# Optimization experiments

Hardware: AMD Instinct MI355X
Metric: run time of the kernel (lower is better)

## Reference

```python
import jax, jax.numpy as jnp
import numpy as np
from jax import lax

DIM = 128
DIM_PREV = 64
DIM_NEXT = 256
HEADS = 4
HID = int(DIM * 2.66)  # 340
B, H, W = 8, 128, 128


def conv2d(x, w, stride=1, pad=0, groups=1):
    return lax.conv_general_dilated(
        x, w, (stride, stride), ((pad, pad), (pad, pad)),
        feature_group_count=groups,
        dimension_numbers=('NCHW', 'OIHW', 'NCHW'))


def layernorm_c(x, w, b):
    # WithBias LayerNorm over channel dim (unbiased=False var), eps=1e-5
    mu = x.mean(axis=1, keepdims=True)
    var = ((x - mu) ** 2).mean(axis=1, keepdims=True)
    return (x - mu) / jnp.sqrt(var + 1e-5) * w[None, :, None, None] + b[None, :, None, None]


def pixel_shuffle(x, r=2):
    b, c, h, w = x.shape
    co = c // (r * r)
    return x.reshape(b, co, r, r, h, w).transpose(0, 1, 4, 2, 5, 3).reshape(b, co, h * r, w * r)


def attention(x, temperature, qkv_w, qkv_dw_w, proj_w, heads):
    b, c, h, w = x.shape
    qkv = conv2d(conv2d(x, qkv_w), qkv_dw_w, pad=1, groups=3 * c)
    q, k, v = jnp.split(qkv, 3, axis=1)
    rs = lambda t: t.reshape(b, heads, c // heads, h * w)
    q, k, v = rs(q), rs(k), rs(v)
    q = q / jnp.maximum(jnp.linalg.norm(q, axis=-1, keepdims=True), 1e-12)
    k = k / jnp.maximum(jnp.linalg.norm(k, axis=-1, keepdims=True), 1e-12)
    # channel-wise attention: [b, heads, c/h, c/h]
    attn = jax.nn.softmax(jnp.einsum('bhcn,bhdn->bhcd', q, k) * temperature[None], axis=-1)
    out = jnp.einsum('bhcd,bhdn->bhcn', attn, v).reshape(b, c, h, w)
    return conv2d(out, proj_w)


def ffn(x, pin_w, dw_w, pout_w):
    x = conv2d(x, pin_w)
    x = conv2d(x, dw_w, pad=1, groups=x.shape[1])
    x1, x2 = jnp.split(x, 2, axis=1)
    return conv2d(jax.nn.gelu(x1, approximate=False) * x2, pout_w)


def setup_inputs() -> dict:
    key = jax.random.key(0)
    ks = jax.random.split(key, 16)
    s = 0.05
    return {
        'x_main': jax.random.normal(ks[0], (B, DIM, H, W), jnp.float32),
        'x_prev': jax.random.normal(ks[1], (B, DIM_PREV, 2 * H, 2 * W), jnp.float32),
        'x_next': jax.random.normal(ks[2], (B, DIM_NEXT, H // 2, W // 2), jnp.float32),
        'alpha_down': jnp.float32(0.5),
        'alpha_up': jnp.float32(0.5),
        'down_w': jax.random.normal(ks[3], (DIM, DIM_PREV, 3, 3), jnp.float32) * s,
        'up_w': jax.random.normal(ks[4], (DIM * 4, DIM_NEXT, 1, 1), jnp.float32) * s,
        'norm1_w': jnp.ones((DIM,), jnp.float32),
        'norm1_b': jnp.zeros((DIM,), jnp.float32),
        'temperature': jnp.ones((HEADS, 1, 1), jnp.float32),
        'qkv_w': jax.random.normal(ks[5], (3 * DIM, DIM, 1, 1), jnp.float32) * s,
        'qkv_dw_w': jax.random.normal(ks[6], (3 * DIM, 1, 3, 3), jnp.float32) * s,
        'proj_w': jax.random.normal(ks[7], (DIM, DIM, 1, 1), jnp.float32) * s,
        'norm2_w': jnp.ones((DIM,), jnp.float32),
        'norm2_b': jnp.zeros((DIM,), jnp.float32),
        'ffn_in_w': jax.random.normal(ks[8], (2 * HID, DIM, 1, 1), jnp.float32) * s,
        'ffn_dw_w': jax.random.normal(ks[9], (2 * HID, 1, 3, 3), jnp.float32) * s,
        'ffn_out_w': jax.random.normal(ks[10], (DIM, HID, 1, 1), jnp.float32) * s,
    }


def reference(x_main, x_prev, x_next, alpha_down, alpha_up, down_w, up_w,
              norm1_w, norm1_b, temperature, qkv_w, qkv_dw_w, proj_w,
              norm2_w, norm2_b, ffn_in_w, ffn_dw_w, ffn_out_w):
    f = x_main + alpha_down * conv2d(x_prev, down_w, stride=2, pad=1)
    f = f + alpha_up * pixel_shuffle(conv2d(x_next, up_w))
    x = attention(layernorm_c(f, norm1_w, norm1_b), temperature, qkv_w, qkv_dw_w, proj_w, HEADS)
    x = x_main + x
    x = x + ffn(layernorm_c(x, norm2_w, norm2_b), ffn_in_w, ffn_dw_w, ffn_out_w)
    return x
```

## Files before the change

### kernel.cpp

```cpp
#include <hip/hip_runtime.h>
#include <hip/hip_bf16.h>
#include <math.h>

using bf16 = __hip_bfloat16;
#define DEV static __device__ __forceinline__

typedef float    fx4   __attribute__((ext_vector_type(4)));
typedef float    fx2   __attribute__((ext_vector_type(2)));
typedef short    s16x8 __attribute__((ext_vector_type(8)));
typedef short    s16x4 __attribute__((ext_vector_type(4)));
typedef __bf16   bfx8  __attribute__((ext_vector_type(8)));
typedef unsigned int u32x4 __attribute__((ext_vector_type(4)));

constexpr int BATCH = 8;
constexpr int NPIX  = 16384;
constexpr int KFF   = 352;
constexpr int MFI   = 768;
constexpr int H1S   = 704;

DEV float uu2f(unsigned short u) { return __uint_as_float(((unsigned)u) << 16); }
DEV unsigned short f2us(float f) { bf16 h = __float2bfloat16(f); return *(unsigned short*)&h; }
DEV float bl2f(bf16 v) { return __bfloat162float(v); }

constexpr size_t OFF_SL1   = 0;
constexpr size_t OFF_XNEXT = OFF_SL1;
constexpr size_t OFF_UP    = OFF_SL1 + 16777216;
constexpr size_t OFF_XPREV = OFF_SL1 + 50331648;
constexpr size_t SZ_SL1    = 184549376;
constexpr size_t OFF_SL2   = OFF_SL1 + SZ_SL1;
constexpr size_t OFF_SL3   = OFF_SL2 + 100663296;
constexpr size_t OFF_SL4   = OFF_SL3 + 33554432;
constexpr size_t OFF_SL5   = OFF_SL4 + 33554432;
constexpr size_t OFF_W     = OFF_SL5 + 33554432;
constexpr size_t OFF_WUP   = OFF_W;
constexpr size_t OFF_WQKV  = OFF_W +  262144;
constexpr size_t OFF_WPRJ  = OFF_W +  360448;
constexpr size_t OFF_WFIN  = OFF_W +  393216;
constexpr size_t OFF_WFOUT = OFF_W +  589824;
constexpr size_t OFF_WTAP  = OFF_W +  679936;
constexpr size_t OFF_ZP    = OFF_W +  827392;
constexpr size_t OFF_NBUF  = OFF_W +  974848;
constexpr size_t OFF_S     = OFF_W +  983040;

__global__ void conv_pad(const float* __restrict__ src, bf16* __restrict__ dst,
                         int Rs, int Cs, int Rd, int Cd)
{
    int n = Rd * Cd;
    for (int i = blockIdx.x * 256 + threadIdx.x; i < n; i += gridDim.x * 256) {
        int r = i / Cd, c = i % Cd;
        dst[i] = (r < Rs && c < Cs) ? __float2bfloat16(src[r * Cs + c]) : bf16(0.f);
    }
}

__global__ void wtap_prep(const float* __restrict__ src, bf16* __restrict__ dst)
{
    int i = blockIdx.x * 256 + threadIdx.x;
    if (i >= 9 * 128 * 64) return;
    int tap = i >> 13, rm = i & 8191, co = rm >> 6, ci = rm & 63;
    dst[i] = __float2bfloat16(src[(co * 64 + ci) * 9 + tap]);
}

__global__ void h1_padzero(bf16* __restrict__ h1)
{
    size_t idx = (size_t)blockIdx.x * 256 + threadIdx.x;
    if (idx >= (size_t)BATCH * NPIX * 24) return;
    size_t n = idx / 24;
    int j = (int)(idx % 24);
    int col = (j < 12) ? 340 + j : 680 + j;
    h1[n * H1S + col] = bf16(0.f);
}

__global__ __launch_bounds__(256) void transpose_c2p(
    const float* __restrict__ in, bf16* __restrict__ out, int C, int HW)
{
    __shared__ float ts[32][33];
    int hw0 = blockIdx.x * 32, c0 = blockIdx.y * 32, b = blockIdx.z;
    int rl = threadIdx.x >> 5, cl = threadIdx.x & 31;
#pragma unroll
    for (int i = 0; i < 4; i++)
        ts[rl + i * 8][cl] = in[((size_t)b * C + c0 + rl + i * 8) * HW + hw0 + cl];
    __syncthreads();
#pragma unroll
    for (int i = 0; i < 4; i++)
        out[((size_t)b * HW + hw0 + rl + i * 8) * C + c0 + cl] =
            __float2bfloat16(ts[cl][rl + i * 8]);
}

template <int EPI>
__global__ __launch_bounds__(256) void gemm_mfma(
    const bf16* __restrict__ Act, const bf16* __restrict__ Wt,
    int K, int Npb, int Mtrue, int Mstride,
    bf16* __restrict__ outB,
    const float* __restrict__ xmain, bf16* __restrict__ x_out,
    const float* __restrict__ nw, const float* __restrict__ nb,
    const bf16* __restrict__ xres, float* __restrict__ outF)
{
    __shared__ short As[128 * 32];
    __shared__ short Bs[128 * 32];
    const int t = threadIdx.x;
    const int w = t >> 6, lane = t & 63;
    const int wr = w >> 1, wc = w & 1;
    const int lr = lane & 15, lg = lane >> 4;
    const int n0 = blockIdx.x * 128;
    const int m0 = blockIdx.y * 128;
    const int b  = blockIdx.z;
    const bf16* Abase = Act + (size_t)b * Npb * K;

    fx4 acc[4][4];
#pragma unroll
    for (int i = 0; i < 4; i++)
#pragma unroll
        for (int j = 0; j < 4; j++) acc[i][j] = fx4{0.f, 0.f, 0.f, 0.f};

    const int f0 = w * 128 + lane, f1 = f0 + 64;
    const int r0 = f0 >> 2, c0 = (f0 & 3) * 8;
    const int r1 = f1 >> 2, c1 = (f1 & 3) * 8;

    for (int ks = 0; ks < K; ks += 32) {
        __builtin_amdgcn_global_load_lds(
            (const __attribute__((address_space(1))) void*)(Abase + (size_t)(n0 + r0) * K + ks + c0),
            (__attribute__((address_space(3))) void*)(As + w * 1024), 16, 0, 0);
        __builtin_amdgcn_global_load_lds(
            (const __attribute__((address_space(1))) void*)(Abase + (size_t)(n0 + r1) * K + ks + c1),
            (__attribute__((address_space(3))) void*)(As + w * 1024 + 512), 16, 0, 0);
        __builtin_amdgcn_global_load_lds(
            (const __attribute__((address_space(1))) void*)(Wt + (size_t)(m0 + r0) * K + ks + c0),
            (__attribute__((address_space(3))) void*)(Bs + w * 1024), 16, 0, 0);
        __builtin_amdgcn_global_load_lds(
            (const __attribute__((address_space(1))) void*)(Wt + (size_t)(m0 + r1) * K + ks + c1),
            (__attribute__((address_space(3))) void*)(Bs + w * 1024 + 512), 16, 0, 0);
        __syncthreads();
        bfx8 af[4], bw[4];
#pragma unroll
        for (int mi = 0; mi < 4; mi++)
            af[mi] = __builtin_bit_cast(bfx8,
                *(const s16x8*)&As[(wr * 64 + mi * 16 + lr) * 32 + lg * 8]);
#pragma unroll
        for (int ni = 0; ni < 4; ni++)
            bw[ni] = __builtin_bit_cast(bfx8,
                *(const s16x8*)&Bs[(wc * 64 + ni * 16 + lr) * 32 + lg * 8]);
#pragma unroll
        for (int mi = 0; mi < 4; mi++)
#pragma unroll
            for (int ni = 0; ni < 4; ni++)
                acc[mi][ni] = __builtin_amdgcn_mfma_f32_16x16x32_bf16(
                    af[mi], bw[ni], acc[mi][ni], 0, 0, 0);
        __syncthreads();
    }

    if (EPI == 0) {
#pragma unroll
        for (int mi = 0; mi < 4; mi++)
#pragma unroll
            for (int ni = 0; ni < 4; ni++) {
                int co = m0 + wc * 64 + ni * 16 + lr;
                if (co < Mtrue) {
#pragma unroll
                    for (int r = 0; r < 4; r++) {
                        int px = n0 + wr * 64 + mi * 16 + lg * 4 + r;
                        outB[((size_t)b * Npb + px) * Mstride + co] =
                            __float2bfloat16(acc[mi][ni][r]);
                    }
                }
            }
    } else if (EPI == 1) {
        float xv[4][4][4];
#pragma unroll
        for (int mi = 0; mi < 4; mi++)
#pragma unroll
            for (int ni = 0; ni < 4; ni++) {
                int co = wc * 64 + ni * 16 + lr;
                fx4 x4 = *(const fx4*)&xmain[((size_t)b * 128 + co) * 16384 +
                                             n0 + wr * 64 + mi * 16 + lg * 4];
#pragma unroll
                for (int r = 0; r < 4; r++) xv[mi][ni][r] = x4[r] + acc[mi][ni][r];
            }
        __shared__ float ps[2][128];
        __shared__ float pss[2][128];
#pragma unroll
        for (int mi = 0; mi < 4; mi++)
#pragma unroll
            for (int r = 0; r < 4; r++) {
                float s = 0.f, s2 = 0.f;
#pragma unroll
                for (int ni = 0; ni < 4; ni++) {
                    float v = xv[mi][ni][r]; s += v; s2 += v * v;
                }
#pragma unroll
                for (int m = 1; m < 16; m <<= 1) {
                    s  += __shfl_xor(s, m);
                    s2 += __shfl_xor(s2, m);
                }
                if (lr == 0) {
                    int row = wr * 64 + mi * 16 + lg * 4 + r;
                    ps[wc][row] = s; pss[wc][row] = s2;
                }
            }
        __syncthreads();
        float nwv[4], nbv[4];
#pragma unroll
        for (int ni = 0; ni < 4; ni++) {
            int co = wc * 64 + ni * 16 + lr;
            nwv[ni] = nw[co]; nbv[ni] = nb[co];
        }
#pragma unroll
        for (int mi = 0; mi < 4; mi++)
#pragma unroll
            for (int r = 0; r < 4; r++) {
                int row = wr * 64 + mi * 16 + lg * 4 + r;
                float s  = ps[0][row] + ps[1][row];
                float s2 = pss[0][row] + pss[1][row];
                float mu = s * (1.f / 128.f);
                float var = s2 * (1.f / 128.f) - mu * mu;
                float rstd = rsqrtf(var + 1e-5f);
                size_t px = (size_t)b * 16384 + n0 + row;
#pragma unroll
                for (int ni = 0; ni < 4; ni++) {
                    int co = wc * 64 + ni * 16 + lr;
                    float v = xv[mi][ni][r];
                    x_out[px * 128 + co] = __float2bfloat16(v);
                    outB[px * 128 + co] = __float2bfloat16((v - mu) * rstd * nwv[ni] + nbv[ni]);
                }
            }
    } else {
#pragma unroll
        for (int mi = 0; mi < 4; mi++)
#pragma unroll
            for (int ni = 0; ni < 4; ni++) {
                int co = wc * 64 + ni * 16 + lr;
                int pxb = n0 + wr * 64 + mi * 16 + lg * 4;
                fx4 o;
#pragma unroll
                for (int r = 0; r < 4; r++)
                    o[r] = acc[mi][ni][r] +
                           bl2f(xres[((size_t)b * 16384 + pxb + r) * 128 + co]);
                *(fx4*)&outF[((size_t)b * 128 + co) * 16384 + pxb] = o;
            }
    }
}

template <int REMAP>
__global__ __launch_bounds__(256) void gemm_mloop(
    const bf16* __restrict__ Act, const bf16* __restrict__ Wt,
    int nM, int Mtrue, int Mstride, bf16* __restrict__ outB)
{
    __shared__ short As[16384];
    __shared__ short Bs[16384];
    const int t = threadIdx.x;
    const int w = t >> 6, lane = t & 63;
    const int wr = w >> 1, wc = w & 1;
    const int lr = lane & 15, lg = lane >> 4;
    const int n0 = blockIdx.x * 128;
    const int b  = blockIdx.y;
    const short* Abase = (const short*)Act + (size_t)b * NPIX * 128;

#pragma unroll
    for (int i = 0; i < 8; i++) {
        int chunk = i * 256 + w * 64 + lane;
        int kb = chunk >> 9, row = (chunk >> 2) & 127, c8 = chunk & 3;
        __builtin_amdgcn_global_load_lds(
            (const __attribute__((address_space(1))) void*)
                (Abase + (size_t)(n0 + row) * 128 + kb * 32 + c8 * 8),
            (__attribute__((address_space(3))) void*)(As + i * 2048 + w * 512), 16, 0, 0);
    }

    for (int mt = 0; mt < nM; mt++) {
#pragma unroll
        for (int i = 0; i < 8; i++) {
            int chunk = i * 256 + w * 64 + lane;
            int kb = chunk >> 9, row = (chunk >> 2) & 127, c8 = chunk & 3;
            __builtin_amdgcn_global_load_lds(
                (const __attribute__((address_space(1))) void*)
                    ((const short*)Wt + (size_t)(mt * 128 + row) * 128 + kb * 32 + c8 * 8),
                (__attribute__((address_space(3))) void*)(Bs + i * 2048 + w * 512), 16, 0, 0);
        }
        __syncthreads();
        fx4 acc[4][4];
#pragma unroll
        for (int i = 0; i < 4; i++)
#pragma unroll
            for (int j = 0; j < 4; j++) acc[i][j] = fx4{0.f, 0.f, 0.f, 0.f};
#pragma unroll
        for (int ks = 0; ks < 4; ks++) {
            bfx8 af[4], bw[4];
#pragma unroll
            for (int mi = 0; mi < 4; mi++)
                af[mi] = __builtin_bit_cast(bfx8,
                    *(const s16x8*)&As[ks * 4096 + (wr * 64 + mi * 16 + lr) * 32 + lg * 8]);
#pragma unroll
            for (int ni = 0; ni < 4; ni++)
                bw[ni] = __builtin_bit_cast(bfx8,
                    *(const s16x8*)&Bs[ks * 4096 + (wc * 64 + ni * 16 + lr) * 32 + lg * 8]);
#pragma unroll
            for (int mi = 0; mi < 4; mi++)
#pragma unroll
                for (int ni = 0; ni < 4; ni++)
                    acc[mi][ni] = __builtin_amdgcn_mfma_f32_16x16x32_bf16(
                        af[mi], bw[ni], acc[mi][ni], 0, 0, 0);
        }
        __syncthreads();
#pragma unroll
        for (int mi = 0; mi < 4; mi++)
#pragma unroll
            for (int ni = 0; ni < 4; ni++) {
                int co = mt * 128 + wc * 64 + ni * 16 + lr;
                if (co < Mtrue) {
                    int cd = (REMAP && co >= 340) ? co + 12 : co;
#pragma unroll
                    for (int r = 0; r < 4; r++) {
                        int px = n0 + wr * 64 + mi * 16 + lg * 4 + r;
                        outB[((size_t)b * NPIX + px) * Mstride + cd] =
                            __float2bfloat16(acc[mi][ni][r]);
                    }
                }
            }
    }
}

__global__ __launch_bounds__(256) void down_mfma_ln(
    const bf16* __restrict__ xprev_pm,
    const float* __restrict__ xmain,
    const bf16* __restrict__ up_pm,
    const bf16* __restrict__ wtap,
    const float* __restrict__ alpha_d, const float* __restrict__ alpha_u,
    const float* __restrict__ n1w, const float* __restrict__ n1b,
    const bf16* __restrict__ zeropage,
    bf16* __restrict__ y1)
{
    __shared__ short As[128 * 64];
    __shared__ short Bs[128 * 64];
    __shared__ float ps[2][128];
    __shared__ float pss[2][128];
    const int t = threadIdx.x;
    const int w = t >> 6, lane = t & 63;
    const int wr = w >> 1, wc = w & 1;
    const int lr = lane & 15, lg = lane >> 4;
    const int y = blockIdx.x;
    const int b = blockIdx.y;

    const int srow0 = 32 * w + (lane >> 3);
    const int sci8  = lane & 7;
    const short* wtbase = (const short*)wtap;

    fx4 acc[4][4];
#pragma unroll
    for (int i = 0; i < 4; i++)
#pragma unroll
        for (int j = 0; j < 4; j++) acc[i][j] = fx4{0.f, 0.f, 0.f, 0.f};

#pragma unroll
    for (int tap = 0; tap < 9; tap++) {
        const int dy = tap / 3, dx = tap % 3;
        const int iy = 2 * y - 1 + dy;
        const bool rowok = (iy >= 0) && (iy < 256);
        const short* arow = (const short*)xprev_pm +
                            (((size_t)b * 65536 + (size_t)iy * 256) * 64);
#pragma unroll
        for (int i = 0; i < 4; i++) {
            int row = srow0 + 8 * i;
            int ix = 2 * row - 1 + dx;
            const short* src = (rowok && ix >= 0 && ix < 256)
                                 ? (arow + (size_t)ix * 64 + sci8 * 8)
                                 : (const short*)zeropage;
            __builtin_amdgcn_global_load_lds(
                (const __attribute__((address_space(1))) void*)src,
                (__attribute__((address_space(3))) void*)(As + w * 2048 + i * 512), 16, 0, 0);
            __builtin_amdgcn_global_load_lds(
                (const __attribute__((address_space(1))) void*)
                    (wtbase + tap * 8192 + w * 2048 + i * 512 + lane * 8),
                (__attribute__((address_space(3))) void*)(Bs + w * 2048 + i * 512), 16, 0, 0);
        }
        __syncthreads();
        bfx8 af[4][2], bw[4][2];
#pragma unroll
        for (int mi = 0; mi < 4; mi++)
#pragma unroll
            for (int ks = 0; ks < 2; ks++)
                af[mi][ks] = __builtin_bit_cast(bfx8,
                    *(const s16x8*)&As[(wr * 64 + mi * 16 + lr) * 64 + ks * 32 + lg * 8]);
#pragma unroll
        for (int ni = 0; ni < 4; ni++)
#pragma unroll
            for (int ks = 0; ks < 2; ks++)
                bw[ni][ks] = __builtin_bit_cast(bfx8,
                    *(const s16x8*)&Bs[(wc * 64 + ni * 16 + lr) * 64 + ks * 32 + lg * 8]);
#pragma unroll
        for (int mi = 0; mi < 4; mi++)
#pragma unroll
            for (int ni = 0; ni < 4; ni++)
#pragma unroll
                for (int ks = 0; ks < 2; ks++)
                    acc[mi][ni] = __builtin_amdgcn_mfma_f32_16x16x32_bf16(
                        af[mi][ks], bw[ni][ks], acc[mi][ni], 0, 0, 0);
        __syncthreads();
    }

    const float ad = alpha_d[0], au = alpha_u[0];
    const int n2base = (y >> 1) * 64;
    const int chb2 = (y & 1) * 2;
    float fv[4][4][4];
#pragma unroll
    for (int mi = 0; mi < 4; mi++) {
        const int x0 = wr * 64 + mi * 16 + lg * 4;
#pragma unroll
        for (int ni = 0; ni < 4; ni++) {
            const int co = wc * 64 + ni * 16 + lr;
            fx4 xm = *(const fx4*)&xmain[(((size_t)b * 128 + co) * 128 + y) * 128 + x0];
            const short* uprow = (const short*)up_pm +
                ((size_t)b * 4096 + n2base + (x0 >> 1)) * 512 + co * 4 + chb2;
            unsigned up01 = *(const unsigned*)uprow;
            unsigned up23 = *(const unsigned*)(uprow + 512);
            fv[mi][ni][0] = xm[0] + ad * acc[mi][ni][0] + au * uu2f((unsigned short)(up01 & 0xffff));
            fv[mi][ni][1] = xm[1] + ad * acc[mi][ni][1] + au * uu2f((unsigned short)(up01 >> 16));
            fv[mi][ni][2] = xm[2] + ad * acc[mi][ni][2] + au * uu2f((unsigned short)(up23 & 0xffff));
            fv[mi][ni][3] = xm[3] + ad * acc[mi][ni][3] + au * uu2f((unsigned short)(up23 >> 16));
        }
    }
#pragma unroll
    for (int mi = 0; mi < 4; mi++)
#pragma unroll
        for (int r = 0; r < 4; r++) {
            float s = 0.f, s2 = 0.f;
#pragma unroll
            for (int ni = 0; ni < 4; ni++) {
                float v = fv[mi][ni][r]; s += v; s2 += v * v;
            }
#pragma unroll
            for (int m = 1; m < 16; m <<= 1) {
                s  += __shfl_xor(s, m);
                s2 += __shfl_xor(s2, m);
            }
            if (lr == 0) {
                int row = wr * 64 + mi * 16 + lg * 4 + r;
                ps[wc][row] = s; pss[wc][row] = s2;
            }
        }
    __syncthreads();
    float nwv[4], nbv[4];
#pragma unroll
    for (int ni = 0; ni < 4; ni++) {
        int co = wc * 64 + ni * 16 + lr;
        nwv[ni] = n1w[co]; nbv[ni] = n1b[co];
    }
#pragma unroll
    for (int mi = 0; mi < 4; mi++)
#pragma unroll
        for (int r = 0; r < 4; r++) {
            int row = wr * 64 + mi * 16 + lg * 4 + r;
            float s  = ps[0][row] + ps[1][row];
            float s2 = pss[0][row] + pss[1][row];
            float mu = s * (1.f / 128.f);
            float var = s2 * (1.f / 128.f) - mu * mu;
            float rstd = rsqrtf(var + 1e-5f);
            size_t px = (size_t)b * 16384 + (size_t)y * 128 + row;
#pragma unroll
            for (int ni = 0; ni < 4; ni++) {
                int co = wc * 64 + ni * 16 + lr;
                ((short*)y1)[px * 128 + co] =
                    (short)f2us((fv[mi][ni][r] - mu) * rstd * nwv[ni] + nbv[ni]);
            }
        }
}

DEV void dw_accum(const short* __restrict__ L, const float* __restrict__ swb,
                  int x, int yh, int lofs, fx2 acc[4][4])
{
    fx2 wreg[9][4];
#pragma unroll
    for (int tap = 0; tap < 9; tap++)
#pragma unroll
        for (int k = 0; k < 4; k++)
            wreg[tap][k] = *(const fx2*)&swb[tap * 32 + lofs + 2 * k];
#pragma unroll
    for (int yy = 0; yy < 4; yy++)
#pragma unroll
        for (int k = 0; k < 4; k++) acc[yy][k] = fx2{0.f, 0.f};
#pragma unroll
    for (int r = 0; r < 6; r++) {
        fx2 rv[3][4];
#pragma unroll
        for (int dxp = 0; dxp < 3; dxp++) {
            s16x8 raw = *(const s16x8*)&L[((yh * 4 + r) * 34 + x + dxp) * 40 + lofs];
            u32x4 u = __builtin_bit_cast(u32x4, raw);
#pragma unroll
            for (int k = 0; k < 4; k++)
                rv[dxp][k] = fx2{__uint_as_float(u[k] << 16),
                                 __uint_as_float(u[k] & 0xffff0000u)};
        }
#pragma unroll
        for (int yy = 0; yy < 4; yy++) {
            int dy = r - yy;
            if (dy < 0 || dy > 2) continue;
#pragma unroll
            for (int dx = 0; dx < 3; dx++)
#pragma unroll
                for (int k = 0; k < 4; k++)
                    acc[yy][k] += rv[dx][k] * wreg[dy * 3 + dx][k];
        }
    }
}

template <int GATE, int QKNORM>
__global__ __launch_bounds__(256) void dw_conv(
    const bf16* __restrict__ in, const float* __restrict__ w,
    bf16* __restrict__ out, float* __restrict__ nbuf)
{
    constexpr int CHST  = GATE ? 704 : 384;
    constexpr int CHOST = GATE ? 352 : 384;
    __shared__ short L1[13600];
    __shared__ short L2[GATE ? 13600 : 8];
    __shared__ float sw1[288];
    __shared__ float sw2[GATE ? 288 : 8];
    __shared__ float snorm[32];
    const int t = threadIdx.x;
    const int x = t & 31, chg = (t >> 5) & 3, yh = t >> 7;
    const int cg = blockIdx.y, b = blockIdx.z;
    const int x0 = (blockIdx.x & 3) * 32, y0 = (blockIdx.x >> 2) * 8;

    if (QKNORM && t < 32) snorm[t] = 0.f;
    if (GATE) {
        for (int i = t; i < 288; i += 256) {
            int c = i & 31, tap = i >> 5;
            int cr = cg * 32 + c;
            sw1[i] = (cr < 340) ? w[cr * 9 + tap] : 0.f;
            sw2[i] = (cr < 340) ? w[(cr + 340) * 9 + tap] : 0.f;
        }
    } else {
        for (int i = t; i < 288; i += 256) {
            int c = i & 31, tap = i >> 5;
            sw1[i] = w[(cg * 32 + c) * 9 + tap];
        }
    }
    const short* bin = (const short*)in + (size_t)b * NPIX * CHST + cg * 32;
    const int NCHK = GATE ? 2720 : 1360;
    for (int id = t; id < NCHK; id += 256) {
        int half = 0, idd = id;
        if (GATE && idd >= 1360) { half = 1; idd -= 1360; }
        int row = idd / 136, rm = idd % 136, pos = rm >> 2, c8 = rm & 3;
        int gy = y0 - 1 + row, gx = x0 - 1 + pos;
        s16x8 v = s16x8{0, 0, 0, 0, 0, 0, 0, 0};
        if (gy >= 0 && gy < 128 && gx >= 0 && gx < 128)
            v = *(const s16x8*)(bin + ((size_t)(gy << 7) + gx) * CHST + half * 352 + c8 * 8);
        short* dst = (GATE && half) ? L2 : L1;
        *(s16x8*)&dst[(row * 34 + pos) * 40 + c8 * 8] = v;
    }
    __syncthreads();

    const int lofs = chg * 8;
    fx2 a1[4][4];
    dw_accum(L1, sw1, x, yh, lofs, a1);
    if (GATE) {
#pragma unroll
        for (int yy = 0; yy < 4; yy++)
#pragma unroll
            for (int k = 0; k < 4; k++) {
                fx2 v = a1[yy][k];
#pragma unroll
                for (int e = 0; e < 2; e++) {
                    float xx = v[e];
                    float x2 = xx * xx;
                    float mzz = xx * fmaf(-0.1029432f, x2, -2.3022082f);
                    float un = exp2f(mzz);
                    v[e] = xx * __builtin_amdgcn_rcpf(1.f + un);
                }
                a1[yy][k] = v;
            }
        fx2 a2[4][4];
        dw_accum(L2, sw2, x, yh, lofs, a2);
#pragma unroll
        for (int yy = 0; yy < 4; yy++)
#pragma unroll
            for (int k = 0; k < 4; k++) a1[yy][k] *= a2[yy][k];
    }

    if (QKNORM && cg < 8) {
        fx2 sq[4];
#pragma unroll
        for (int k = 0; k < 4; k++) {
            sq[k] = fx2{0.f, 0.f};
#pragma unroll
            for (int yy = 0; yy < 4; yy++) sq[k] += a1[yy][k] * a1[yy][k];
        }
#pragma unroll
        for (int m = 1; m < 32; m <<= 1)
#pragma unroll
            for (int k = 0; k < 4; k++) {
                sq[k][0] += __shfl_xor(sq[k][0], m);
                sq[k][1] += __shfl_xor(sq[k][1], m);
            }
        if (x == 0) {
#pragma unroll
            for (int k = 0; k < 4; k++) {
                atomicAdd(&snorm[chg * 8 + 2 * k],     sq[k][0]);
                atomicAdd(&snorm[chg * 8 + 2 * k + 1], sq[k][1]);
            }
        }
    }

#pragma unroll
    for (int yy = 0; yy < 4; yy++) {
        s16x8 pk;
#pragma unroll
        for (int k = 0; k < 4; k++) {
            pk[2 * k]     = (short)f2us(a1[yy][k][0]);
            pk[2 * k + 1] = (short)f2us(a1[yy][k][1]);
        }
        *(s16x8*)((short*)out + (((size_t)b * NPIX) + ((y0 + yh * 4 + yy) << 7) + x0 + x) * CHOST
                  + cg * 32 + chg * 8) = pk;
    }

    if (QKNORM) {
        __syncthreads();
        if (cg < 8 && t < 32)
            atomicAdd(&nbuf[b * 256 + cg * 32 + t], snorm[t]);
    }
}

__global__ __launch_bounds__(256) void scores(const bf16* __restrict__ qkv,
                                              float* __restrict__ S)
{
    __shared__ short qs[256 * 40];
    __shared__ short ks2[256 * 40];
    const int t = threadIdx.x;
    const int bh = blockIdx.x, b = bh >> 2, h = bh & 3;
    const int n0 = blockIdx.y * 256;
    {
        const short* src = (const short*)qkv + ((size_t)(b * 16384 + n0 + t)) * 384 + h * 32;
#pragma unroll
        for (int i = 0; i < 4; i++) {
            *(s16x8*)&qs[t * 40 + i * 8]  = *(const s16x8*)(src + i * 8);
            *(s16x8*)&ks2[t * 40 + i * 8] = *(const s16x8*)(src + 128 + i * 8);
        }
    }
    __syncthreads();
    const int i2 = t >> 4, j16 = t & 15;
    float a00 = 0.f, a01 = 0.f, a10 = 0.f, a11 = 0.f;
    for (int n = 0; n < 256; n++) {
        unsigned qq = *(const unsigned*)&qs[n * 40 + i2 * 2];
        unsigned kk = *(const unsigned*)&ks2[n * 40 + j16 * 2];
        float q0 = uu2f((unsigned short)(qq & 0xffff)), q1 = uu2f((unsigned short)(qq >> 16));
        float k0 = uu2f((unsigned short)(kk & 0xffff)), k1 = uu2f((unsigned short)(kk >> 16));
        a00 = fmaf(q0, k0, a00); a01 = fmaf(q0, k1, a01);
        a10 = fmaf(q1, k0, a10); a11 = fmaf(q1, k1, a11);
    }
    float* base = S + (size_t)bh * 1024;
    atomicAdd(&base[(i2 * 2 + 0) * 32 + j16 * 2 + 0], a00);
    atomicAdd(&base[(i2 * 2 + 0) * 32 + j16 * 2 + 1], a01);
    atomicAdd(&base[(i2 * 2 + 1) * 32 + j16 * 2 + 0], a10);
    atomicAdd(&base[(i2 * 2 + 1) * 32 + j16 * 2 + 1], a11);
}

__global__ void softmax_k(float* __restrict__ S, const float* __restrict__ nbuf,
                          const float* __restrict__ temp)
{
    __shared__ float invk[32];
    int bh = blockIdx.x, b = bh >> 2, h = bh & 3, i = threadIdx.x;
    invk[i] = 1.f / fmaxf(sqrtf(nbuf[b * 256 + 128 + h * 32 + i]), 1e-12f);
    __syncthreads();
    float ti = temp[h] / fmaxf(sqrtf(nbuf[b * 256 + h * 32 + i]), 1e-12f);
    float* row = S + (size_t)bh * 1024 + i * 32;
    float vals[32], m = -1e30f;
#pragma unroll
    for (int j = 0; j < 32; j++) { vals[j] = row[j] * ti * invk[j]; m = fmaxf(m, vals[j]); }
    float s = 0.f;
#pragma unroll
    for (int j = 0; j < 32; j++) { vals[j] = expf(vals[j] - m); s += vals[j]; }
    float r = 1.f / s;
#pragma unroll
    for (int j = 0; j < 32; j++) row[j] = vals[j] * r;
}

__global__ __launch_bounds__(256) void attnapply(const bf16* __restrict__ qkv,
                                                 const float* __restrict__ S,
                                                 bf16* __restrict__ atto)
{
    __shared__ float sa[1024];
    const int t = threadIdx.x;
    const int bh = blockIdx.x, b = bh >> 2, h = bh & 3;
    const int n0 = blockIdx.y * 1024;
    for (int i = t; i < 1024; i += 256) sa[i] = S[(size_t)bh * 1024 + i];
    __syncthreads();
#pragma unroll
    for (int pp = 0; pp < 4; pp++) {
        int n = n0 + (t << 2) + pp;
        const short* vs = (const short*)qkv + ((size_t)(b * 16384) + n) * 384 + 256 + h * 32;
        float v[32];
#pragma unroll
        for (int i = 0; i < 4; i++) {
            s16x8 vv = *(const s16x8*)(vs + i * 8);
#pragma unroll
            for (int e = 0; e < 8; e++) v[i * 8 + e] = uu2f((unsigned short)vv[e]);
        }
        short ov[32];
#pragma unroll
        for (int c = 0; c < 32; c++) {
            const fx4* row = (const fx4*)&sa[c * 32];
            float a = 0.f;
#pragma unroll
            for (int d4 = 0; d4 < 8; d4++) {
                fx4 w4 = row[d4];
                a += w4[0] * v[d4 * 4] + w4[1] * v[d4 * 4 + 1] +
                     w4[2] * v[d4 * 4 + 2] + w4[3] * v[d4 * 4 + 3];
            }
            ov[c] = (short)f2us(a);
        }
        short* dst = (short*)atto + ((size_t)(b * 16384) + n) * 128 + h * 32;
#pragma unroll
        for (int i = 0; i < 4; i++) *(s16x8*)(dst + i * 8) = *(s16x8*)&ov[i * 8];
    }
}

extern "C" void kernel_launch(void* const* d_in, const int* in_sizes, int n_in,
                              void* d_out, int out_size, void* d_ws, size_t ws_size,
                              hipStream_t stream)
{
    const float* x_main      = (const float*)d_in[0];
    const float* x_prev      = (const float*)d_in[1];
    const float* x_next      = (const float*)d_in[2];
    const float* alpha_down  = (const float*)d_in[3];
    const float* alpha_up    = (const float*)d_in[4];
    const float* down_w      = (const float*)d_in[5];
    const float* up_w        = (const float*)d_in[6];
    const float* norm1_w     = (const float*)d_in[7];
    const float* norm1_b     = (const float*)d_in[8];
    const float* temperature = (const float*)d_in[9];
    const float* qkv_w       = (const float*)d_in[10];
    const float* qkv_dw_w    = (const float*)d_in[11];
    const float* proj_w      = (const float*)d_in[12];
    const float* norm2_w     = (const float*)d_in[13];
    const float* norm2_b     = (const float*)d_in[14];
    const float* ffn_in_w    = (const float*)d_in[15];
    const float* ffn_dw_w    = (const float*)d_in[16];
    const float* ffn_out_w   = (const float*)d_in[17];
    float* out = (float*)d_out;
    (void)in_sizes; (void)n_in; (void)out_size; (void)ws_size;

    char* ws = (char*)d_ws;
    bf16* xnext_pm = (bf16*)(ws + OFF_XNEXT);
    bf16* up_pm    = (bf16*)(ws + OFF_UP);
    bf16* xprev_pm = (bf16*)(ws + OFF_XPREV);
    bf16* qkv_a    = (bf16*)(ws + OFF_SL1);
    bf16* h1       = (bf16*)(ws + OFF_SL1);
    bf16* qkv_b    = (bf16*)(ws + OFF_SL2);
    bf16* gbuf     = (bf16*)(ws + OFF_SL2);
    bf16* y1       = (bf16*)(ws + OFF_SL3);
    bf16* atto     = (bf16*)(ws + OFF_SL3);
    bf16* x_pm     = (bf16*)(ws + OFF_SL4);
    bf16* y2       = (bf16*)(ws + OFF_SL5);
    bf16* Wup      = (bf16*)(ws + OFF_WUP);
    bf16* Wqkv     = (bf16*)(ws + OFF_WQKV);
    bf16* Wprj     = (bf16*)(ws + OFF_WPRJ);
    bf16* Wfin     = (bf16*)(ws + OFF_WFIN);
    bf16* Wfout    = (bf16*)(ws + OFF_WFOUT);
    bf16* Wtap     = (bf16*)(ws + OFF_WTAP);
    bf16* zpage    = (bf16*)(ws + OFF_ZP);
    float* nbuf    = (float*)(ws + OFF_NBUF);
    float* Sbuf    = (float*)(ws + OFF_S);

    hipMemsetAsync(nbuf, 0, 8192 + 131072, stream);
    hipMemsetAsync(zpage, 0, 256, stream);

    conv_pad<<<dim3(512), 256, 0, stream>>>(up_w, Wup, 512, 256, 512, 256);
    conv_pad<<<dim3(192), 256, 0, stream>>>(qkv_w, Wqkv, 384, 128, 384, 128);
    conv_pad<<<dim3(64), 256, 0, stream>>>(proj_w, Wprj, 128, 128, 128, 128);
    conv_pad<<<dim3(384), 256, 0, stream>>>(ffn_in_w, Wfin, 680, 128, MFI, 128);
    conv_pad<<<dim3(176), 256, 0, stream>>>(ffn_out_w, Wfout, 128, 340, 128, KFF);
    wtap_prep<<<dim3(288), 256, 0, stream>>>(down_w, Wtap);

    transpose_c2p<<<dim3(128, 8, BATCH), 256, 0, stream>>>(x_next, xnext_pm, 256, 4096);
    transpose_c2p<<<dim3(2048, 2, BATCH), 256, 0, stream>>>(x_prev, xprev_pm, 64, 65536);

    gemm_mfma<0><<<dim3(32, 4, BATCH), 256, 0, stream>>>(
        xnext_pm, Wup, 256, 4096, 512, 512, up_pm,
        nullptr, nullptr, nullptr, nullptr, nullptr, nullptr);

    down_mfma_ln<<<dim3(128, BATCH), 256, 0, stream>>>(
        xprev_pm, x_main, up_pm, Wtap, alpha_down, alpha_up, norm1_w, norm1_b,
        zpage, y1);

    gemm_mloop<0><<<dim3(128, BATCH), 256, 0, stream>>>(y1, Wqkv, 3, 384, 384, qkv_a);

    dw_conv<0, 1><<<dim3(64, 12, BATCH), 256, 0, stream>>>(qkv_a, qkv_dw_w, qkv_b, nbuf);

    scores<<<dim3(32, 64), 256, 0, stream>>>(qkv_b, Sbuf);
    softmax_k<<<dim3(32), 32, 0, stream>>>(Sbuf, nbuf, temperature);
    attnapply<<<dim3(32, 16), 256, 0, stream>>>(qkv_b, Sbuf, atto);

    gemm_mfma<1><<<dim3(128, 1, BATCH), 256, 0, stream>>>(
        atto, Wprj, 128, NPIX, 128, 128, y2,
        x_main, x_pm, norm2_w, norm2_b, nullptr, nullptr);

    h1_padzero<<<dim3((BATCH * NPIX * 24 + 255) / 256), 256, 0, stream>>>(h1);
    gemm_mloop<1><<<dim3(128, BATCH), 256, 0, stream>>>(y2, Wfin, 6, 680, H1S, h1);

    dw_conv<1, 0><<<dim3(64, 11, BATCH), 256, 0, stream>>>(h1, ffn_dw_w, gbuf, nullptr);

    gemm_mfma<2><<<dim3(128, 1, BATCH), 256, 0, stream>>>(
        gbuf, Wfout, KFF, NPIX, 128, 128, nullptr,
        nullptr, nullptr, nullptr, nullptr, x_pm, out);
}
```

Measured before the change: 615.7 us.

## Fold attention matrix into projection weights and trim FFN staging

```diff
diff --git a/kernel.cpp b/kernel.cpp
--- a/kernel.cpp
+++ b/kernel.cpp
@@ -41,6 +41,7 @@
 constexpr size_t OFF_ZP    = OFF_W +  827392;
 constexpr size_t OFF_NBUF  = OFF_W +  974848;
 constexpr size_t OFF_S     = OFF_W +  983040;
+constexpr size_t OFF_W2    = OFF_W + 1114112;
 
 __global__ void conv_pad(const float* __restrict__ src, bf16* __restrict__ dst,
                          int Rs, int Cs, int Rd, int Cd)
@@ -60,16 +61,6 @@
     dst[i] = __float2bfloat16(src[(co * 64 + ci) * 9 + tap]);
 }
 
-__global__ void h1_padzero(bf16* __restrict__ h1)
-{
-    size_t idx = (size_t)blockIdx.x * 256 + threadIdx.x;
-    if (idx >= (size_t)BATCH * NPIX * 24) return;
-    size_t n = idx / 24;
-    int j = (int)(idx % 24);
-    int col = (j < 12) ? 340 + j : 680 + j;
-    h1[n * H1S + col] = bf16(0.f);
-}
-
 __global__ __launch_bounds__(256) void transpose_c2p(
     const float* __restrict__ in, bf16* __restrict__ out, int C, int HW)
 {
@@ -89,7 +80,7 @@
 template <int EPI>
 __global__ __launch_bounds__(256) void gemm_mfma(
     const bf16* __restrict__ Act, const bf16* __restrict__ Wt,
-    int K, int Npb, int Mtrue, int Mstride,
+    int K, int Npb, int Mtrue, int Mstride, int Astride, int Aoff, int WtBS,
     bf16* __restrict__ outB,
     const float* __restrict__ xmain, bf16* __restrict__ x_out,
     const float* __restrict__ nw, const float* __restrict__ nb,
@@ -104,7 +95,8 @@
     const int n0 = blockIdx.x * 128;
     const int m0 = blockIdx.y * 128;
     const int b  = blockIdx.z;
-    const bf16* Abase = Act + (size_t)b * Npb * K;
+    const bf16* Abase = Act + (size_t)b * Npb * Astride + Aoff;
+    const bf16* Wtb   = Wt + (size_t)b * WtBS;
 
     fx4 acc[4][4];
 #pragma unroll
@@ -118,16 +110,16 @@
 
     for (int ks = 0; ks < K; ks += 32) {
         __builtin_amdgcn_global_load_lds(
-            (const __attribute__((address_space(1))) void*)(Abase + (size_t)(n0 + r0) * K + ks + c0),
+            (const __attribute__((address_space(1))) void*)(Abase + (size_t)(n0 + r0) * Astride + ks + c0),
             (__attribute__((address_space(3))) void*)(As + w * 1024), 16, 0, 0);
         __builtin_amdgcn_global_load_lds(
-            (const __attribute__((address_space(1))) void*)(Abase + (size_t)(n0 + r1) * K + ks + c1),
+            (const __attribute__((address_space(1))) void*)(Abase + (size_t)(n0 + r1) * Astride + ks + c1),
             (__attribute__((address_space(3))) void*)(As + w * 1024 + 512), 16, 0, 0);
         __builtin_amdgcn_global_load_lds(
-            (const __attribute__((address_space(1))) void*)(Wt + (size_t)(m0 + r0) * K + ks + c0),
+            (const __attribute__((address_space(1))) void*)(Wtb + (size_t)(m0 + r0) * K + ks + c0),
             (__attribute__((address_space(3))) void*)(Bs + w * 1024), 16, 0, 0);
         __builtin_amdgcn_global_load_lds(
-            (const __attribute__((address_space(1))) void*)(Wt + (size_t)(m0 + r1) * K + ks + c1),
+            (const __attribute__((address_space(1))) void*)(Wtb + (size_t)(m0 + r1) * K + ks + c1),
             (__attribute__((address_space(3))) void*)(Bs + w * 1024 + 512), 16, 0, 0);
         __syncthreads();
         bfx8 af[4], bw[4];
@@ -311,6 +303,19 @@
                         int px = n0 + wr * 64 + mi * 16 + lg * 4 + r;
                         outB[((size_t)b * NPIX + px) * Mstride + cd] =
                             __float2bfloat16(acc[mi][ni][r]);
+                    }
+                    if (REMAP && co >= 340 && co < 352) {
+#pragma unroll
+                        for (int r = 0; r < 4; r++) {
+                            int px = n0 + wr * 64 + mi * 16 + lg * 4 + r;
+                            outB[((size_t)b * NPIX + px) * Mstride + co] = bf16(0.f);
+                        }
+                    }
+                } else if (REMAP && co < 692) {
+#pragma unroll
+                    for (int r = 0; r < 4; r++) {
+                        int px = n0 + wr * 64 + mi * 16 + lg * 4 + r;
+                        outB[((size_t)b * NPIX + px) * Mstride + co + 12] = bf16(0.f);
                     }
                 }
             }
@@ -465,53 +470,48 @@
 DEV void dw_accum(const short* __restrict__ L, const float* __restrict__ swb,
                   int x, int yh, int lofs, fx2 acc[4][4])
 {
-    fx2 wreg[9][4];
-#pragma unroll
-    for (int tap = 0; tap < 9; tap++)
-#pragma unroll
-        for (int k = 0; k < 4; k++)
-            wreg[tap][k] = *(const fx2*)&swb[tap * 32 + lofs + 2 * k];
 #pragma unroll
     for (int yy = 0; yy < 4; yy++)
 #pragma unroll
         for (int k = 0; k < 4; k++) acc[yy][k] = fx2{0.f, 0.f};
 #pragma unroll
-    for (int r = 0; r < 6; r++) {
-        fx2 rv[3][4];
-#pragma unroll
-        for (int dxp = 0; dxp < 3; dxp++) {
-            s16x8 raw = *(const s16x8*)&L[((yh * 4 + r) * 34 + x + dxp) * 40 + lofs];
+    for (int dxp = 0; dxp < 3; dxp++) {
+        fx2 rv[6][4];
+#pragma unroll
+        for (int r = 0; r < 6; r++) {
+            s16x8 raw = *(const s16x8*)&L[((yh * 4 + r) * 34 + x + dxp) * 44 + lofs];
             u32x4 u = __builtin_bit_cast(u32x4, raw);
 #pragma unroll
             for (int k = 0; k < 4; k++)
-                rv[dxp][k] = fx2{__uint_as_float(u[k] << 16),
-                                 __uint_as_float(u[k] & 0xffff0000u)};
-        }
-#pragma unroll
-        for (int yy = 0; yy < 4; yy++) {
-            int dy = r - yy;
-            if (dy < 0 || dy > 2) continue;
-#pragma unroll
-            for (int dx = 0; dx < 3; dx++)
+                rv[r][k] = fx2{__uint_as_float(u[k] << 16),
+                               __uint_as_float(u[k] & 0xffff0000u)};
+        }
+#pragma unroll
+        for (int dy = 0; dy < 3; dy++) {
+            fx2 wv[4];
+#pragma unroll
+            for (int k = 0; k < 4; k++)
+                wv[k] = *(const fx2*)&swb[(dy * 3 + dxp) * 32 + lofs + 2 * k];
+#pragma unroll
+            for (int yy = 0; yy < 4; yy++)
 #pragma unroll
                 for (int k = 0; k < 4; k++)
-                    acc[yy][k] += rv[dx][k] * wreg[dy * 3 + dx][k];
+                    acc[yy][k] += rv[yy + dy][k] * wv[k];
         }
     }
 }
 
 template <int GATE, int QKNORM>
-__global__ __launch_bounds__(256) void dw_conv(
+__global__ __launch_bounds__(256, 4) void dw_conv(
     const bf16* __restrict__ in, const float* __restrict__ w,
     bf16* __restrict__ out, float* __restrict__ nbuf)
 {
     constexpr int CHST  = GATE ? 704 : 384;
     constexpr int CHOST = GATE ? 352 : 384;
-    __shared__ short L1[13600];
-    __shared__ short L2[GATE ? 13600 : 8];
+    __shared__ short L[10 * 34 * 44];
     __shared__ float sw1[288];
     __shared__ float sw2[GATE ? 288 : 8];
-    __shared__ float snorm[32];
+    __shared__ float snorm[QKNORM ? 32 : 8];
     const int t = threadIdx.x;
     const int x = t & 31, chg = (t >> 5) & 3, yh = t >> 7;
     const int cg = blockIdx.y, b = blockIdx.z;
@@ -532,45 +532,51 @@
         }
     }
     const short* bin = (const short*)in + (size_t)b * NPIX * CHST + cg * 32;
-    const int NCHK = GATE ? 2720 : 1360;
-    for (int id = t; id < NCHK; id += 256) {
-        int half = 0, idd = id;
-        if (GATE && idd >= 1360) { half = 1; idd -= 1360; }
-        int row = idd / 136, rm = idd % 136, pos = rm >> 2, c8 = rm & 3;
-        int gy = y0 - 1 + row, gx = x0 - 1 + pos;
-        s16x8 v = s16x8{0, 0, 0, 0, 0, 0, 0, 0};
-        if (gy >= 0 && gy < 128 && gx >= 0 && gx < 128)
-            v = *(const s16x8*)(bin + ((size_t)(gy << 7) + gx) * CHST + half * 352 + c8 * 8);
-        short* dst = (GATE && half) ? L2 : L1;
-        *(s16x8*)&dst[(row * 34 + pos) * 40 + c8 * 8] = v;
-    }
+    auto stage = [&](int hofs) {
+        for (int id = t; id < 1360; id += 256) {
+            int row = id / 136, rm = id % 136, pos = rm >> 2, c8 = rm & 3;
+            int gy = y0 - 1 + row, gx = x0 - 1 + pos;
+            s16x8 v = s16x8{0, 0, 0, 0, 0, 0, 0, 0};
+            if (gy >= 0 && gy < 128 && gx >= 0 && gx < 128)
+                v = *(const s16x8*)(bin + ((size_t)(gy << 7) + gx) * CHST + hofs + c8 * 8);
+            *(s16x8*)&L[(row * 34 + pos) * 44 + c8 * 8] = v;
+        }
+    };
+    stage(0);
     __syncthreads();
 
     const int lofs = chg * 8;
     fx2 a1[4][4];
-    dw_accum(L1, sw1, x, yh, lofs, a1);
+    dw_accum(L, sw1, x, yh, lofs, a1);
+
     if (GATE) {
+        s16x8 p1[4];
 #pragma unroll
         for (int yy = 0; yy < 4; yy++)
 #pragma unroll
             for (int k = 0; k < 4; k++) {
-                fx2 v = a1[yy][k];
 #pragma unroll
                 for (int e = 0; e < 2; e++) {
-                    float xx = v[e];
+                    float xx = a1[yy][k][e];
                     float x2 = xx * xx;
                     float mzz = xx * fmaf(-0.1029432f, x2, -2.3022082f);
                     float un = exp2f(mzz);
-                    v[e] = xx * __builtin_amdgcn_rcpf(1.f + un);
+                    p1[yy][2 * k + e] = (short)f2us(xx * __builtin_amdgcn_rcpf(1.f + un));
                 }
-                a1[yy][k] = v;
-            }
+            }
+        __syncthreads();
+        stage(352);
+        __syncthreads();
         fx2 a2[4][4];
-        dw_accum(L2, sw2, x, yh, lofs, a2);
+        dw_accum(L, sw2, x, yh, lofs, a2);
 #pragma unroll
         for (int yy = 0; yy < 4; yy++)
 #pragma unroll
-            for (int k = 0; k < 4; k++) a1[yy][k] *= a2[yy][k];
+            for (int k = 0; k < 4; k++) {
+                fx2 g = fx2{uu2f((unsigned short)p1[yy][2 * k]),
+                            uu2f((unsigned short)p1[yy][2 * k + 1])};
+                a1[yy][k] = g * a2[yy][k];
+            }
     }
 
     if (QKNORM && cg < 8) {
@@ -670,44 +676,38 @@
     for (int j = 0; j < 32; j++) row[j] = vals[j] * r;
 }
 
-__global__ __launch_bounds__(256) void attnapply(const bf16* __restrict__ qkv,
-                                                 const float* __restrict__ S,
-                                                 bf16* __restrict__ atto)
-{
-    __shared__ float sa[1024];
-    const int t = threadIdx.x;
-    const int bh = blockIdx.x, b = bh >> 2, h = bh & 3;
-    const int n0 = blockIdx.y * 1024;
-    for (int i = t; i < 1024; i += 256) sa[i] = S[(size_t)bh * 1024 + i];
+__global__ __launch_bounds__(256) void attn_fold(
+    const bf16* __restrict__ Wprj, const float* __restrict__ S, bf16* __restrict__ W2)
+{
+    __shared__ float sS[4096];
+    const int b = blockIdx.x, t = threadIdx.x;
+    for (int i = t; i < 4096; i += 256) sS[i] = S[b * 4096 + i];
     __syncthreads();
-#pragma unroll
-    for (int pp = 0; pp < 4; pp++) {
-        int n = n0 + (t << 2) + pp;
-        const short* vs = (const short*)qkv + ((size_t)(b * 16384) + n) * 384 + 256 + h * 32;
-        float v[32];
-#pragma unroll
-        for (int i = 0; i < 4; i++) {
-            s16x8 vv = *(const s16x8*)(vs + i * 8);
-#pragma unroll
-            for (int e = 0; e < 8; e++) v[i * 8 + e] = uu2f((unsigned short)vv[e]);
-        }
-        short ov[32];
-#pragma unroll
-        for (int c = 0; c < 32; c++) {
-            const fx4* row = (const fx4*)&sa[c * 32];
+    const int co = t >> 1, jh = t & 1;
+    const short* prow = (const short*)Wprj + co * 128 + jh * 64;
+    float p[64];
+#pragma unroll
+    for (int i = 0; i < 8; i++) {
+        s16x8 v = *(const s16x8*)(prow + i * 8);
+#pragma unroll
+        for (int e = 0; e < 8; e++) p[i * 8 + e] = uu2f((unsigned short)v[e]);
+    }
+    short outv[64];
+#pragma unroll
+    for (int h2 = 0; h2 < 2; h2++) {
+        const int h = jh * 2 + h2;
+        const float* Sh = &sS[h * 1024];
+#pragma unroll 4
+        for (int d = 0; d < 32; d++) {
             float a = 0.f;
 #pragma unroll
-            for (int d4 = 0; d4 < 8; d4++) {
-                fx4 w4 = row[d4];
-                a += w4[0] * v[d4 * 4] + w4[1] * v[d4 * 4 + 1] +
-                     w4[2] * v[d4 * 4 + 2] + w4[3] * v[d4 * 4 + 3];
-            }
-            ov[c] = (short)f2us(a);
-        }
-        short* dst = (short*)atto + ((size_t)(b * 16384) + n) * 128 + h * 32;
-#pragma unroll
-        for (int i = 0; i < 4; i++) *(s16x8*)(dst + i * 8) = *(s16x8*)&ov[i * 8];
-    }
+            for (int c = 0; c < 32; c++) a = fmaf(p[h2 * 32 + c], Sh[c * 32 + d], a);
+            outv[h2 * 32 + d] = (short)f2us(a);
+        }
+    }
+    short* dst = (short*)W2 + (size_t)b * 16384 + co * 128 + jh * 64;
+#pragma unroll
+    for (int i = 0; i < 8; i++) *(s16x8*)(dst + i * 8) = *(s16x8*)&outv[i * 8];
 }
 
 extern "C" void kernel_launch(void* const* d_in, const int* in_sizes, int n_in,
@@ -744,7 +744,6 @@
     bf16* qkv_b    = (bf16*)(ws + OFF_SL2);
     bf16* gbuf     = (bf16*)(ws + OFF_SL2);
     bf16* y1       = (bf16*)(ws + OFF_SL3);
-    bf16* atto     = (bf16*)(ws + OFF_SL3);
     bf16* x_pm     = (bf16*)(ws + OFF_SL4);
     bf16* y2       = (bf16*)(ws + OFF_SL5);
     bf16* Wup      = (bf16*)(ws + OFF_WUP);
@@ -756,6 +755,7 @@
     bf16* zpage    = (bf16*)(ws + OFF_ZP);
     float* nbuf    = (float*)(ws + OFF_NBUF);
     float* Sbuf    = (float*)(ws + OFF_S);
+    bf16* W2buf    = (bf16*)(ws + OFF_W2);
 
     hipMemsetAsync(nbuf, 0, 8192 + 131072, stream);
     hipMemsetAsync(zpage, 0, 256, stream);
@@ -771,7 +771,7 @@
     transpose_c2p<<<dim3(2048, 2, BATCH), 256, 0, stream>>>(x_prev, xprev_pm, 64, 65536);
 
     gemm_mfma<0><<<dim3(32, 4, BATCH), 256, 0, stream>>>(
-        xnext_pm, Wup, 256, 4096, 512, 512, up_pm,
+        xnext_pm, Wup, 256, 4096, 512, 512, 256, 0, 0, up_pm,
         nullptr, nullptr, nullptr, nullptr, nullptr, nullptr);
 
     down_mfma_ln<<<dim3(128, BATCH), 256, 0, stream>>>(
@@ -784,18 +784,17 @@
 
     scores<<<dim3(32, 64), 256, 0, stream>>>(qkv_b, Sbuf);
     softmax_k<<<dim3(32), 32, 0, stream>>>(Sbuf, nbuf, temperature);
-    attnapply<<<dim3(32, 16), 256, 0, stream>>>(qkv_b, Sbuf, atto);
+    attn_fold<<<dim3(BATCH), 256, 0, stream>>>(Wprj, Sbuf, W2buf);
 
     gemm_mfma<1><<<dim3(128, 1, BATCH), 256, 0, stream>>>(
-        atto, Wprj, 128, NPIX, 128, 128, y2,
+        qkv_b, W2buf, 128, NPIX, 128, 128, 384, 256, 16384, y2,
         x_main, x_pm, norm2_w, norm2_b, nullptr, nullptr);
 
-    h1_padzero<<<dim3((BATCH * NPIX * 24 + 255) / 256), 256, 0, stream>>>(h1);
     gemm_mloop<1><<<dim3(128, BATCH), 256, 0, stream>>>(y2, Wfin, 6, 680, H1S, h1);
 
     dw_conv<1, 0><<<dim3(64, 11, BATCH), 256, 0, stream>>>(h1, ffn_dw_w, gbuf, nullptr);
 
     gemm_mfma<2><<<dim3(128, 1, BATCH), 256, 0, stream>>>(
-        gbuf, Wfout, KFF, NPIX, 128, 128, nullptr,
+        gbuf, Wfout, KFF, NPIX, 128, 128, KFF, 0, 0, nullptr,
         nullptr, nullptr, nullptr, nullptr, x_pm, out);
 }
```

Result: slower. 800.4 us (+30.0%).
